# Performance work log

Measured on AMD Instinct MI355X. Metric: run time of the kernel, lower is better.

The kernel has to match this reference:

```python
import jax, jax.numpy as jnp
import numpy as np

UNITS = 80
LATENT = 128
IN_DIM = 256
BATCH = 8192
SIZE = 256


def _lstm_zero_state_step(x, K, b):
    """One Keras LSTM step from zero (h0, c0). activation=relu, recurrent_activation=sigmoid.
    With h0=0 the recurrent kernel contributes nothing; with c0=0 the forget gate is inert.
    Keras gate order in kernel/bias: i, f, c, o."""
    z = x @ K + b                       # (B, 4*UNITS)
    zi, zf, zc, zo = jnp.split(z, 4, axis=-1)
    c = jax.nn.sigmoid(zi) * jax.nn.relu(zc)   # i * act(c_tilde)
    return jax.nn.sigmoid(zo) * jax.nn.relu(c) # o * act(c)


def setup_inputs() -> dict:
    key = jax.random.key(0)
    ks = jax.random.split(key, 9)
    s = 0.05
    return {
        "x": jax.random.normal(ks[0], (BATCH, IN_DIM), jnp.float32),
        "size": SIZE,
        "W_lat": jax.random.normal(ks[1], (IN_DIM, LATENT), jnp.float32) * s,
        "b_lat": jax.random.normal(ks[2], (LATENT,), jnp.float32) * s,
        "K_fw": jax.random.normal(ks[3], (LATENT, 4 * UNITS), jnp.float32) * s,
        "b_fw": jax.random.normal(ks[4], (4 * UNITS,), jnp.float32) * s,
        "K_bw": jax.random.normal(ks[5], (LATENT, 4 * UNITS), jnp.float32) * s,
        "b_bw": jax.random.normal(ks[6], (4 * UNITS,), jnp.float32) * s,
        "K_1": jax.random.normal(ks[7], (2 * UNITS, 4 * UNITS), jnp.float32) * s,
        "b_1": jax.random.normal(ks[8], (4 * UNITS,), jnp.float32) * s,
    }


def reference(x, size, W_lat, b_lat, K_fw, b_fw, K_bw, b_bw, K_1, b_1):
    # Dense latent projection
    lat = x @ W_lat + b_lat                      # (B, 128)

    def decode_step(inp):                        # inp: (B, 128)
        # Bidirectional over a length-1 sequence: fw and bw both see the same
        # single timestep; merge mode is concat([forward, backward]).
        h_fw = _lstm_zero_state_step(inp, K_fw, b_fw)
        h_bw = _lstm_zero_state_step(inp, K_bw, b_bw)
        h = jnp.concatenate([h_fw, h_bw], axis=-1)   # (B, 160)
        return _lstm_zero_state_step(h, K_1, b_1)    # (B, 80)

    # The original Python loop feeds the latent vector only on iteration 0;
    # every later iteration feeds tf.ones(x_shape), and all Keras layers are
    # stateless (fresh zero state each call), so steps 1..size-1 are identical.
    y0 = decode_step(lat)                         # (B, 80)
    yc = decode_step(jnp.ones_like(lat))          # (B, 80)
    B = x.shape[0]
    rest = jnp.broadcast_to(yc[:, None, :], (B, size - 1, UNITS))
    return jnp.concatenate([y0[:, None, :], rest], axis=1)  # (B, size, 80)
```

## Files before the change

### kernel.cpp

```cpp
#include <hip/hip_runtime.h>
#include <math.h>

#define UNITS 80
#define LATENT 128
#define IN_DIM 256
#define BATCH 8192
#define SEQ 256
#define G 320
#define H2 160

#define TPB 640
#define RPB 4
#define NBLK (BATCH / RPB)

typedef float f4 __attribute__((ext_vector_type(4)));

__device__ __forceinline__ float sigf(float v) {
    return 1.0f / (1.0f + __expf(-v));
}

__global__ __launch_bounds__(640)
void yc_kernel(const float* __restrict__ Kf, const float* __restrict__ bf,
               const float* __restrict__ Kb, const float* __restrict__ bb,
               const float* __restrict__ K1, const float* __restrict__ b1,
               float* __restrict__ yc) {
    __shared__ float z[2 * G];
    __shared__ float h[H2];
    const int t = threadIdx.x;

    {
        const float* K   = (t < G) ? Kf : Kb;
        const float* bia = (t < G) ? bf : bb;
        const int c = (t < G) ? t : t - G;
        float acc = bia[c];
#pragma unroll 8
        for (int l = 0; l < LATENT; ++l) acc += K[l * G + c];
        z[t] = acc;
    }
    __syncthreads();
    if (t < UNITS) {
        h[t] = sigf(z[240 + t]) * sigf(z[t]) * fmaxf(z[160 + t], 0.f);
    } else if (t >= G && t < G + UNITS) {
        const int u = t - G;
        h[UNITS + u] = sigf(z[G + 240 + u]) * sigf(z[G + u]) * fmaxf(z[G + 160 + u], 0.f);
    }
    __syncthreads();
    if (t < G) {
        float acc = b1[t];
#pragma unroll 8
        for (int l = 0; l < H2; ++l) acc = fmaf(h[l], K1[l * G + t], acc);
        z[t] = acc;
    }
    __syncthreads();
    if (t < UNITS) yc[t] = sigf(z[240 + t]) * sigf(z[t]) * fmaxf(z[160 + t], 0.f);
}

__global__ __launch_bounds__(TPB)
void main_kernel(const float* __restrict__ x,
                 const float* __restrict__ Wl, const float* __restrict__ bl,
                 const float* __restrict__ Kf, const float* __restrict__ bf,
                 const float* __restrict__ Kb, const float* __restrict__ bb,
                 const float* __restrict__ K1, const float* __restrict__ b1,
                 const float* __restrict__ yc,
                 float* __restrict__ out) {
    __shared__ float xs[RPB * IN_DIM];
    __shared__ float lat_s[RPB * LATENT];
    __shared__ float h_s[RPB * H2];
    __shared__ f4 yc4s[UNITS / 4];

    const int t = threadIdx.x;
    const int R0 = blockIdx.x * RPB;

    if (t < UNITS / 4) yc4s[t] = ((const f4*)yc)[t];
    {
        const f4* xg = (const f4*)(x + (size_t)R0 * IN_DIM);
        f4* xs4 = (f4*)xs;
        if (t < RPB * IN_DIM / 4) xs4[t] = xg[t];
    }
    __syncthreads();

    {
        const f4 yv = yc4s[t % (UNITS / 4)];
        f4* out4 = (f4*)out;
        const int per_row = (SEQ - 1) * UNITS / 4;
#pragma unroll
        for (int r = 0; r < RPB; ++r) {
            f4* rowp = out4 + (size_t)(R0 + r) * (SEQ * UNITS / 4) + (UNITS / 4);
#pragma unroll
            for (int k = 0; k < 8; ++k) {
                const int j = t + k * TPB;
                if (j < per_row) __builtin_nontemporal_store(yv, rowp + j);
            }
        }
    }

    if (t < 512) {
        const int row = t >> 7, col = t & 127;
        float acc = bl[col];
        const float* xr = xs + row * IN_DIM;
#pragma unroll 8
        for (int l = 0; l < IN_DIM; ++l) acc = fmaf(xr[l], Wl[l * LATENT + col], acc);
        lat_s[row * LATENT + col] = acc;
    }
    __syncthreads();

    {
        const int half = t / G;
        const int tt = t - half * G;
        const int row = tt / UNITS;
        const int u = tt - row * UNITS;
        const float* K   = half ? Kb : Kf;
        const float* bia = half ? bb : bf;
        float ai = 0.f, ac = 0.f, ao = 0.f;
        const float* lr = lat_s + row * LATENT;
#pragma unroll 4
        for (int k = 0; k < LATENT; ++k) {
            const float lv = lr[k];
            ai = fmaf(lv, K[k * G + u], ai);
            ac = fmaf(lv, K[k * G + 160 + u], ac);
            ao = fmaf(lv, K[k * G + 240 + u], ao);
        }
        h_s[row * H2 + half * UNITS + u] =
            sigf(ao + bia[240 + u]) * sigf(ai + bia[u]) * fmaxf(ac + bia[160 + u], 0.f);
    }
    __syncthreads();

    if (t < G) {
        const int row = t / UNITS;
        const int u = t - row * UNITS;
        float ai = 0.f, ac = 0.f, ao = 0.f;
        const float* hr = h_s + row * H2;
#pragma unroll 4
        for (int k = 0; k < H2; ++k) {
            const float hv = hr[k];
            ai = fmaf(hv, K1[k * G + u], ai);
            ac = fmaf(hv, K1[k * G + 160 + u], ac);
            ao = fmaf(hv, K1[k * G + 240 + u], ao);
        }
        const float y = sigf(ao + b1[240 + u]) * sigf(ai + b1[u]) * fmaxf(ac + b1[160 + u], 0.f);
        __builtin_nontemporal_store(y, out + (size_t)(R0 + row) * SEQ * UNITS + u);
    }
}

extern "C" void kernel_launch(void* const* d_in, const int* in_sizes, int n_in,
                              void* d_out, int out_size, void* d_ws, size_t ws_size,
                              hipStream_t stream) {
    const float* x   = (const float*)d_in[0];
    const float* Wl  = (const float*)d_in[2];
    const float* bl  = (const float*)d_in[3];
    const float* Kf  = (const float*)d_in[4];
    const float* bf  = (const float*)d_in[5];
    const float* Kb  = (const float*)d_in[6];
    const float* bb  = (const float*)d_in[7];
    const float* K1  = (const float*)d_in[8];
    const float* b1  = (const float*)d_in[9];
    float* out = (float*)d_out;
    float* yc  = (float*)d_ws;

    yc_kernel<<<1, 640, 0, stream>>>(Kf, bf, Kb, bb, K1, b1, yc);
    main_kernel<<<NBLK, TPB, 0, stream>>>(x, Wl, bl, Kf, bf, Kb, bb, K1, b1, yc, out);
}
```

Before: 201.5 us.

## Process 16 rows per block and defer broadcast stores until after compute

Raises rows per block from 4 to 16 and turns the fixed thread-to-work mapping into strided loops, so each block reuses the weight reads from cache over more rows and there are fewer blocks. The output stores now happen at the end, after the compute phases, and the y0 row is written together with the broadcast fill from a shared staging buffer. This removes the scattered scalar store and the early store flood that used to compete with the compute loads. In exchange the block uses more shared memory and has fewer blocks to hide latency with, and the stores no longer overlap the compute.

```diff
diff --git a/kernel.cpp b/kernel.cpp
--- a/kernel.cpp
+++ b/kernel.cpp
@@ -8,9 +8,10 @@
 #define SEQ 256
 #define G 320
 #define H2 160
+#define ROW_F4 (SEQ * UNITS / 4)
 
 #define TPB 640
-#define RPB 4
+#define RPB 16
 #define NBLK (BATCH / RPB)
 
 typedef float f4 __attribute__((ext_vector_type(4)));
@@ -66,52 +67,37 @@
     __shared__ float xs[RPB * IN_DIM];
     __shared__ float lat_s[RPB * LATENT];
     __shared__ float h_s[RPB * H2];
-    __shared__ f4 yc4s[UNITS / 4];
+    __shared__ float y_s[RPB * UNITS];
 
     const int t = threadIdx.x;
     const int R0 = blockIdx.x * RPB;
 
-    if (t < UNITS / 4) yc4s[t] = ((const f4*)yc)[t];
+    const f4 yv = ((const f4*)yc)[t % (UNITS / 4)];
+
     {
         const f4* xg = (const f4*)(x + (size_t)R0 * IN_DIM);
-        f4* xs4 = (f4*)xs;
-        if (t < RPB * IN_DIM / 4) xs4[t] = xg[t];
+        for (int i = t; i < RPB * IN_DIM / 4; i += TPB) ((f4*)xs)[i] = xg[i];
     }
     __syncthreads();
 
-    {
-        const f4 yv = yc4s[t % (UNITS / 4)];
-        f4* out4 = (f4*)out;
-        const int per_row = (SEQ - 1) * UNITS / 4;
-#pragma unroll
-        for (int r = 0; r < RPB; ++r) {
-            f4* rowp = out4 + (size_t)(R0 + r) * (SEQ * UNITS / 4) + (UNITS / 4);
-#pragma unroll
-            for (int k = 0; k < 8; ++k) {
-                const int j = t + k * TPB;
-                if (j < per_row) __builtin_nontemporal_store(yv, rowp + j);
-            }
-        }
-    }
-
-    if (t < 512) {
-        const int row = t >> 7, col = t & 127;
+    for (int i = t; i < RPB * LATENT; i += TPB) {
+        const int row = i >> 7, col = i & 127;
         float acc = bl[col];
         const float* xr = xs + row * IN_DIM;
 #pragma unroll 8
         for (int l = 0; l < IN_DIM; ++l) acc = fmaf(xr[l], Wl[l * LATENT + col], acc);
-        lat_s[row * LATENT + col] = acc;
+        lat_s[i] = acc;
     }
     __syncthreads();
 
-    {
-        const int half = t / G;
-        const int tt = t - half * G;
-        const int row = tt / UNITS;
-        const int u = tt - row * UNITS;
+    for (int i = t; i < 2 * RPB * UNITS; i += TPB) {
+        const int half = (i >= RPB * UNITS);
+        const int j = half ? i - RPB * UNITS : i;
+        const int row = j / UNITS;
+        const int u = j - row * UNITS;
         const float* K   = half ? Kb : Kf;
         const float* bia = half ? bb : bf;
-        float ai = 0.f, ac = 0.f, ao = 0.f;
+        float ai = bia[u], ac = bia[160 + u], ao = bia[240 + u];
         const float* lr = lat_s + row * LATENT;
 #pragma unroll 4
         for (int k = 0; k < LATENT; ++k) {
@@ -120,15 +106,14 @@
             ac = fmaf(lv, K[k * G + 160 + u], ac);
             ao = fmaf(lv, K[k * G + 240 + u], ao);
         }
-        h_s[row * H2 + half * UNITS + u] =
-            sigf(ao + bia[240 + u]) * sigf(ai + bia[u]) * fmaxf(ac + bia[160 + u], 0.f);
+        h_s[row * H2 + half * UNITS + u] = sigf(ao) * sigf(ai) * fmaxf(ac, 0.f);
     }
     __syncthreads();
 
-    if (t < G) {
-        const int row = t / UNITS;
-        const int u = t - row * UNITS;
-        float ai = 0.f, ac = 0.f, ao = 0.f;
+    for (int i = t; i < RPB * UNITS; i += TPB) {
+        const int row = i / UNITS;
+        const int u = i - row * UNITS;
+        float ai = b1[u], ac = b1[160 + u], ao = b1[240 + u];
         const float* hr = h_s + row * H2;
 #pragma unroll 4
         for (int k = 0; k < H2; ++k) {
@@ -137,8 +122,23 @@
             ac = fmaf(hv, K1[k * G + 160 + u], ac);
             ao = fmaf(hv, K1[k * G + 240 + u], ao);
         }
-        const float y = sigf(ao + b1[240 + u]) * sigf(ai + b1[u]) * fmaxf(ac + b1[160 + u], 0.f);
-        __builtin_nontemporal_store(y, out + (size_t)(R0 + row) * SEQ * UNITS + u);
+        y_s[i] = sigf(ao) * sigf(ai) * fmaxf(ac, 0.f);
+    }
+    __syncthreads();
+
+    __builtin_amdgcn_sched_barrier(0);
+
+    {
+        f4* out4 = (f4*)out;
+        const f4* ys4 = (const f4*)y_s;
+        for (int r = 0; r < RPB; ++r) {
+            f4* rowp = out4 + (size_t)(R0 + r) * ROW_F4;
+            const f4 v0 = (t < UNITS / 4) ? ys4[r * (UNITS / 4) + t] : yv;
+            __builtin_nontemporal_store(v0, rowp + t);
+#pragma unroll
+            for (int k = 1; k < ROW_F4 / TPB; ++k)
+                __builtin_nontemporal_store(yv, rowp + t + k * TPB);
+        }
     }
 }
 
```

After: 271.8 us. +34.9%, slower.
